# Performance work log

Hardware: AMD Instinct MI355X
Metric: run time of the kernel (lower is better)

The kernel has to match this reference:

```python
import jax, jax.numpy as jnp
import numpy as np

NUM_TAGS = 128
NUM_FEATURES = 500000
B, T, F = 64, 512, 8


def setup_inputs() -> dict:
    key = jax.random.key(0)
    ks = jax.random.split(key, 6)
    feats = jax.random.randint(ks[0], (B, T, F), 0, NUM_FEATURES)
    tags = jax.random.randint(ks[1], (B, T), 0, NUM_TAGS)
    # original init: uniform(-0.01, 0.01)
    state_weights = jax.random.uniform(ks[2], (NUM_TAGS, NUM_FEATURES), minval=-0.01, maxval=0.01, dtype=jnp.float32)
    transitions = jax.random.uniform(ks[3], (NUM_TAGS, NUM_TAGS), minval=-0.01, maxval=0.01, dtype=jnp.float32)
    start_transitions = jax.random.uniform(ks[4], (NUM_TAGS,), minval=-0.01, maxval=0.01, dtype=jnp.float32)
    end_transitions = jax.random.uniform(ks[5], (NUM_TAGS,), minval=-0.01, maxval=0.01, dtype=jnp.float32)
    return dict(feats=feats, tags=tags, state_weights=state_weights,
                transitions=transitions, start_transitions=start_transitions,
                end_transitions=end_transitions)


def reference(feats, tags, state_weights, transitions, start_transitions, end_transitions):
    """Batched CRF negative log-likelihood per sentence: logZ - gold_score. Returns [B]."""
    # emissions[b,t,k] = sum_f state_weights[k, feats[b,t,f]]  (emissions_for_sentence)
    emissions = jnp.take(state_weights, feats, axis=1).sum(-1)   # [K,B,T]
    emissions = jnp.moveaxis(emissions, 0, -1)                    # [B,T,K]

    # log_partition: forward algorithm over T via scan
    alpha0 = start_transitions[None, :] + emissions[:, 0]         # [B,K]

    def step(alpha, em_t):
        # scores[b,i,j] = alpha[b,i] + transitions[i,j]
        scores = alpha[:, :, None] + transitions[None, :, :]
        return jax.nn.logsumexp(scores, axis=1) + em_t, None

    em_rest = jnp.moveaxis(emissions[:, 1:], 1, 0)                # [T-1,B,K]
    alphaT, _ = jax.lax.scan(step, alpha0, em_rest)
    log_z = jax.nn.logsumexp(alphaT + end_transitions[None, :], axis=1)   # [B]

    # gold_score, vectorized over batch
    em_gold = jnp.take_along_axis(emissions, tags[..., None], axis=2)[..., 0].sum(axis=1)  # [B]
    trans_gold = transitions[tags[:, :-1], tags[:, 1:]].sum(axis=1)                        # [B]
    gold = start_transitions[tags[:, 0]] + end_transitions[tags[:, -1]] + em_gold + trans_gold

    return log_z - gold
```

## Files before the change

kernel.cpp:

```cpp
#include <hip/hip_runtime.h>

#define NUM_TAGS 128
#define NUM_FEATS 500000
#define BB 64
#define TT 512
#define FF 8

#define SWT_BYTES 128000000ull
#define EM_BYTES  16777216ull
#define NEED_FULL (SWT_BYTES + EM_BYTES)

typedef __attribute__((ext_vector_type(8))) short short8;
typedef __attribute__((ext_vector_type(4))) float float4v;

__device__ inline unsigned short f2bf(float f) {
  unsigned u = __float_as_uint(f);
  return (unsigned short)((u + 0x7fffu + ((u >> 16) & 1u)) >> 16);
}
__device__ inline float bf2f(unsigned short h) {
  return __uint_as_float(((unsigned)h) << 16);
}

__global__ __launch_bounds__(256) void transpose_kernel(
    const float* __restrict__ sw, unsigned short* __restrict__ swT) {
  __shared__ float tile[32][129];
  const int f0 = blockIdx.x * 32;
  const int t = threadIdx.x;
  const int fi = t & 31, kb = t >> 5;
#pragma unroll
  for (int it = 0; it < 16; ++it) {
    int k = kb + it * 8;
    tile[fi][k] = sw[(size_t)k * NUM_FEATS + f0 + fi];
  }
  __syncthreads();
  const int kp = (t & 63) * 2, fo = t >> 6;
#pragma unroll
  for (int it = 0; it < 8; ++it) {
    int f2 = fo + it * 4;
    unsigned v = (unsigned)f2bf(tile[f2][kp]) |
                 ((unsigned)f2bf(tile[f2][kp + 1]) << 16);
    *(unsigned*)&swT[(size_t)(f0 + f2) * NUM_TAGS + kp] = v;
  }
}

__global__ __launch_bounds__(128) void gather_t_kernel(
    const int* __restrict__ feats, const unsigned short* __restrict__ swT,
    float* __restrict__ em_exp) {
  const int token = blockIdx.x;
  const int k = threadIdx.x;
  const int* f = feats + token * FF;
  float s = 0.f;
#pragma unroll
  for (int i = 0; i < FF; ++i) s += bf2f(swT[(size_t)f[i] * NUM_TAGS + k]);
  em_exp[(size_t)token * NUM_TAGS + k] = __expf(s);
}

__global__ __launch_bounds__(128) void gather_f_kernel(
    const int* __restrict__ feats, const float* __restrict__ sw,
    float* __restrict__ em_exp) {
  const int token = blockIdx.x;
  const int k = threadIdx.x;
  const int* f = feats + token * FF;
  const float* row = sw + (size_t)k * NUM_FEATS;
  float s = 0.f;
#pragma unroll
  for (int i = 0; i < FF; ++i) s += row[f[i]];
  em_exp[(size_t)token * NUM_TAGS + k] = __expf(s);
}

#define NB 16
#define LROW 136
#define LBUF (NB * LROW)

__global__ __launch_bounds__(256, 1) void fwd_kernel(
    const float* __restrict__ em_exp, const int* __restrict__ tags,
    const float* __restrict__ trans, const float* __restrict__ startT,
    const float* __restrict__ endT, float* __restrict__ out) {
  __shared__ __align__(16) unsigned short abuf[2][LBUF];
  __shared__ float red[16][17];

  const int tid = threadIdx.x;
  const int bl = tid & 15;
  const int h = (tid >> 4) & 3;
  const int w = tid >> 6;
  const int bg = blockIdx.x * NB + bl;

  short8 afrag[2][4];
#pragma unroll
  for (int mt = 0; mt < 2; ++mt) {
    const int j = (2 * w + mt) * 16 + bl;
#pragma unroll
    for (int kc = 0; kc < 4; ++kc) {
      short8 a;
#pragma unroll
      for (int jj = 0; jj < 8; ++jj) {
        int i = kc * 32 + h * 8 + jj;
        a[jj] = (short)f2bf(__expf(trans[i * NUM_TAGS + j]) * 0.0078125f);
      }
      afrag[mt][kc] = a;
    }
  }

  const float* emb = em_exp + (size_t)bg * TT * NUM_TAGS;

  {
    const int jc = tid >> 4, j0 = jc * 8;
#pragma unroll
    for (int jj = 0; jj < 8; ++jj)
      abuf[0][bl * LROW + j0 + jj] =
          f2bf(__expf(startT[j0 + jj]) * emb[j0 + jj]);
  }
  __syncthreads();

  float4v ev[2];
#pragma unroll
  for (int mt = 0; mt < 2; ++mt) {
    int j0 = (2 * w + mt) * 16 + h * 4;
    ev[mt] = *(const float4v*)&emb[(size_t)NUM_TAGS + j0];
  }

  for (int t = 1; t < TT; ++t) {
    const unsigned short* cur = abuf[(t - 1) & 1];
    unsigned short* nxt = abuf[t & 1];

    short8 bfrag[4];
#pragma unroll
    for (int kc = 0; kc < 4; ++kc)
      bfrag[kc] = *(const short8*)&cur[bl * LROW + kc * 32 + h * 8];

    float4v acc0 = {0.f, 0.f, 0.f, 0.f}, acc1 = {0.f, 0.f, 0.f, 0.f};
#pragma unroll
    for (int kc = 0; kc < 4; ++kc) {
      acc0 = __builtin_amdgcn_mfma_f32_16x16x32_bf16(afrag[0][kc], bfrag[kc], acc0, 0, 0, 0);
      acc1 = __builtin_amdgcn_mfma_f32_16x16x32_bf16(afrag[1][kc], bfrag[kc], acc1, 0, 0, 0);
    }

    float4v e0 = ev[0], e1 = ev[1];
    if (t + 1 < TT) {
#pragma unroll
      for (int mt = 0; mt < 2; ++mt) {
        int j0 = (2 * w + mt) * 16 + h * 4;
        ev[mt] = *(const float4v*)&emb[(size_t)(t + 1) * NUM_TAGS + j0];
      }
    }
    {
      int j0 = (2 * w + 0) * 16 + h * 4;
      uint2 u;
      u.x = (unsigned)f2bf(acc0[0] * e0[0]) | ((unsigned)f2bf(acc0[1] * e0[1]) << 16);
      u.y = (unsigned)f2bf(acc0[2] * e0[2]) | ((unsigned)f2bf(acc0[3] * e0[3]) << 16);
      *(uint2*)&nxt[bl * LROW + j0] = u;
    }
    {
      int j0 = (2 * w + 1) * 16 + h * 4;
      uint2 u;
      u.x = (unsigned)f2bf(acc1[0] * e1[0]) | ((unsigned)f2bf(acc1[1] * e1[1]) << 16);
      u.y = (unsigned)f2bf(acc1[2] * e1[2]) | ((unsigned)f2bf(acc1[3] * e1[3]) << 16);
      *(uint2*)&nxt[bl * LROW + j0] = u;
    }
    __syncthreads();
  }

  {
    const int jc = tid >> 4, j0 = jc * 8;
    const unsigned short* fin = abuf[(TT - 1) & 1];
    float val = 0.f;
#pragma unroll
    for (int jj = 0; jj < 8; ++jj)
      val += bf2f(fin[bl * LROW + j0 + jj]) * __expf(endT[j0 + jj]);
    red[jc][bl] = val;
  }
  __syncthreads();
  float logzv = 0.f;
  if (tid < 16) {
    float s = 0.f;
#pragma unroll
    for (int q = 0; q < 16; ++q) s += red[q][tid];
    logzv = __logf(s) + 511.0f * 7.0f * 0.69314718055994531f;
  }
  __syncthreads();

  {
    const int seg = tid >> 4;
    const int* tb = tags + (size_t)bg * TT;
    float g = 0.f;
    for (int t = seg * 32; t < seg * 32 + 32; ++t) {
      int tg = tb[t];
      g += __logf(emb[(size_t)t * NUM_TAGS + tg]);
      if (t < TT - 1) g += trans[tg * NUM_TAGS + tb[t + 1]];
    }
    if (seg == 0) g += startT[tb[0]];
    if (seg == 15) g += endT[tb[TT - 1]];
    red[seg][bl] = g;
  }
  __syncthreads();
  if (tid < 16) {
    float s = 0.f;
#pragma unroll
    for (int q = 0; q < 16; ++q) s += red[q][tid];
    out[blockIdx.x * NB + tid] = logzv - s;
  }
}

extern "C" void kernel_launch(void* const* d_in, const int* in_sizes, int n_in,
                              void* d_out, int out_size, void* d_ws, size_t ws_size,
                              hipStream_t stream) {
  const int* feats = (const int*)d_in[0];
  const int* tags = (const int*)d_in[1];
  const float* sw = (const float*)d_in[2];
  const float* trans = (const float*)d_in[3];
  const float* startT = (const float*)d_in[4];
  const float* endT = (const float*)d_in[5];
  float* out = (float*)d_out;

  if (ws_size >= NEED_FULL) {
    unsigned short* swT = (unsigned short*)d_ws;
    float* em_exp = (float*)((char*)d_ws + SWT_BYTES);
    transpose_kernel<<<NUM_FEATS / 32, 256, 0, stream>>>(sw, swT);
    gather_t_kernel<<<BB * TT, 128, 0, stream>>>(feats, swT, em_exp);
    fwd_kernel<<<BB / NB, 256, 0, stream>>>(em_exp, tags, trans, startT, endT, out);
  } else {
    float* em_exp = (float*)d_ws;
    gather_f_kernel<<<BB * TT, 128, 0, stream>>>(feats, sw, em_exp);
    fwd_kernel<<<BB / NB, 256, 0, stream>>>(em_exp, tags, trans, startT, endT, out);
  }
}
```

Baseline: 633.9 us.

## Run CRF forward recursion in one wave with bf16 emissions and vectorized transpose

The forward recursion now runs entirely in a single wavefront that holds all eight MFMA tiles, so the per-timestep __syncthreads across four waves and the LDS double buffer go away. A second wave computes the gold score at the same time. Emissions are stored as bf16 instead of fp32, halving their write and read traffic. The transpose now uses float4 loads, and the gather packs two tags per lane with four tokens per block. Risks are lower emission precision, a longer serial MFMA chain per step in one wave, and cheaper round-to-nearest without ties-to-even in the recurrence.

```diff
diff --git a/kernel.cpp b/kernel.cpp
--- a/kernel.cpp
+++ b/kernel.cpp
@@ -7,7 +7,7 @@
 #define FF 8
 
 #define SWT_BYTES 128000000ull
-#define EM_BYTES  16777216ull
+#define EM_BYTES  (64ull * 512 * 128 * 2)
 #define NEED_FULL (SWT_BYTES + EM_BYTES)
 
 typedef __attribute__((ext_vector_type(8))) short short8;
@@ -23,182 +23,187 @@
 
 __global__ __launch_bounds__(256) void transpose_kernel(
     const float* __restrict__ sw, unsigned short* __restrict__ swT) {
-  __shared__ float tile[32][129];
+  __shared__ float tile[128][33];
   const int f0 = blockIdx.x * 32;
   const int t = threadIdx.x;
-  const int fi = t & 31, kb = t >> 5;
-#pragma unroll
-  for (int it = 0; it < 16; ++it) {
-    int k = kb + it * 8;
-    tile[fi][k] = sw[(size_t)k * NUM_FEATS + f0 + fi];
+  const int c = t & 7, kr = t >> 3;
+#pragma unroll
+  for (int p = 0; p < 4; ++p) {
+    int k = kr + 32 * p;
+    float4 v = *(const float4*)&sw[(size_t)k * NUM_FEATS + f0 + 4 * c];
+    tile[k][4 * c + 0] = v.x; tile[k][4 * c + 1] = v.y;
+    tile[k][4 * c + 2] = v.z; tile[k][4 * c + 3] = v.w;
   }
   __syncthreads();
-  const int kp = (t & 63) * 2, fo = t >> 6;
-#pragma unroll
-  for (int it = 0; it < 8; ++it) {
-    int f2 = fo + it * 4;
-    unsigned v = (unsigned)f2bf(tile[f2][kp]) |
-                 ((unsigned)f2bf(tile[f2][kp + 1]) << 16);
-    *(unsigned*)&swT[(size_t)(f0 + f2) * NUM_TAGS + kp] = v;
-  }
-}
-
-__global__ __launch_bounds__(128) void gather_t_kernel(
+  const int l = t & 63, fr = t >> 6;
+#pragma unroll
+  for (int p = 0; p < 8; ++p) {
+    int f = fr + 4 * p;
+    unsigned lo = f2bf(tile[2 * l][f]);
+    unsigned hi = f2bf(tile[2 * l + 1][f]);
+    *(unsigned*)&swT[(size_t)(f0 + f) * NUM_TAGS + 2 * l] = lo | (hi << 16);
+  }
+}
+
+__global__ __launch_bounds__(256) void gather_kernel(
     const int* __restrict__ feats, const unsigned short* __restrict__ swT,
-    float* __restrict__ em_exp) {
-  const int token = blockIdx.x;
-  const int k = threadIdx.x;
+    unsigned short* __restrict__ em) {
+  const int w = threadIdx.x >> 6, lane = threadIdx.x & 63;
+  const int token = blockIdx.x * 4 + w;
   const int* f = feats + token * FF;
-  float s = 0.f;
-#pragma unroll
-  for (int i = 0; i < FF; ++i) s += bf2f(swT[(size_t)f[i] * NUM_TAGS + k]);
-  em_exp[(size_t)token * NUM_TAGS + k] = __expf(s);
-}
-
-__global__ __launch_bounds__(128) void gather_f_kernel(
+  int fi[FF];
+#pragma unroll
+  for (int i = 0; i < FF; ++i) fi[i] = f[i];
+  float s0 = 0.f, s1 = 0.f;
+#pragma unroll
+  for (int i = 0; i < FF; ++i) {
+    unsigned u = *(const unsigned*)&swT[(size_t)fi[i] * NUM_TAGS + 2 * lane];
+    s0 += __uint_as_float(u << 16);
+    s1 += __uint_as_float(u & 0xFFFF0000u);
+  }
+  unsigned lo = f2bf(__expf(s0));
+  unsigned hi = f2bf(__expf(s1));
+  *(unsigned*)&em[(size_t)token * NUM_TAGS + 2 * lane] = lo | (hi << 16);
+}
+
+__global__ __launch_bounds__(256) void gather_f_kernel(
     const int* __restrict__ feats, const float* __restrict__ sw,
-    float* __restrict__ em_exp) {
-  const int token = blockIdx.x;
-  const int k = threadIdx.x;
+    unsigned short* __restrict__ em) {
+  const int w = threadIdx.x >> 6, lane = threadIdx.x & 63;
+  const int token = blockIdx.x * 4 + w;
   const int* f = feats + token * FF;
-  const float* row = sw + (size_t)k * NUM_FEATS;
-  float s = 0.f;
-#pragma unroll
-  for (int i = 0; i < FF; ++i) s += row[f[i]];
-  em_exp[(size_t)token * NUM_TAGS + k] = __expf(s);
+  float s0 = 0.f, s1 = 0.f;
+#pragma unroll
+  for (int i = 0; i < FF; ++i) {
+    s0 += sw[(size_t)(2 * lane) * NUM_FEATS + f[i]];
+    s1 += sw[(size_t)(2 * lane + 1) * NUM_FEATS + f[i]];
+  }
+  unsigned lo = f2bf(__expf(s0));
+  unsigned hi = f2bf(__expf(s1));
+  *(unsigned*)&em[(size_t)token * NUM_TAGS + 2 * lane] = lo | (hi << 16);
 }
 
 #define NB 16
 #define LROW 136
-#define LBUF (NB * LROW)
-
-__global__ __launch_bounds__(256, 1) void fwd_kernel(
-    const float* __restrict__ em_exp, const int* __restrict__ tags,
+
+__global__ __launch_bounds__(128, 1) void fwd_kernel(
+    const unsigned short* __restrict__ em, const int* __restrict__ tags,
     const float* __restrict__ trans, const float* __restrict__ startT,
     const float* __restrict__ endT, float* __restrict__ out) {
-  __shared__ __align__(16) unsigned short abuf[2][LBUF];
-  __shared__ float red[16][17];
+  __shared__ __align__(16) unsigned short alds[NB * LROW];
+  __shared__ float redz[NB], redg[NB];
 
   const int tid = threadIdx.x;
-  const int bl = tid & 15;
-  const int h = (tid >> 4) & 3;
-  const int w = tid >> 6;
-  const int bg = blockIdx.x * NB + bl;
-
-  short8 afrag[2][4];
-#pragma unroll
-  for (int mt = 0; mt < 2; ++mt) {
-    const int j = (2 * w + mt) * 16 + bl;
-#pragma unroll
-    for (int kc = 0; kc < 4; ++kc) {
-      short8 a;
-#pragma unroll
-      for (int jj = 0; jj < 8; ++jj) {
-        int i = kc * 32 + h * 8 + jj;
-        a[jj] = (short)f2bf(__expf(trans[i * NUM_TAGS + j]) * 0.0078125f);
-      }
-      afrag[mt][kc] = a;
-    }
-  }
-
-  const float* emb = em_exp + (size_t)bg * TT * NUM_TAGS;
-
-  {
-    const int jc = tid >> 4, j0 = jc * 8;
-#pragma unroll
-    for (int jj = 0; jj < 8; ++jj)
-      abuf[0][bl * LROW + j0 + jj] =
-          f2bf(__expf(startT[j0 + jj]) * emb[j0 + jj]);
-  }
+  const int wav = tid >> 6, lane = tid & 63;
+  const int bl = lane & 15, h = lane >> 4;
+  const int b0 = blockIdx.x * NB;
+
+  if (wav == 0) {
+    short8 afrag[8][4];
+#pragma unroll
+    for (int mt = 0; mt < 8; ++mt) {
+      const int j = mt * 16 + bl;
+#pragma unroll
+      for (int kc = 0; kc < 4; ++kc) {
+        short8 a;
+#pragma unroll
+        for (int jj = 0; jj < 8; ++jj) {
+          int i = kc * 32 + h * 8 + jj;
+          a[jj] = (short)f2bf(__expf(trans[i * NUM_TAGS + j]) * 0.0078125f);
+        }
+        afrag[mt][kc] = a;
+      }
+    }
+
+    const unsigned short* emb = em + (size_t)(b0 + bl) * TT * NUM_TAGS;
+
+#pragma unroll
+    for (int mt = 0; mt < 8; ++mt)
+#pragma unroll
+      for (int r = 0; r < 4; ++r) {
+        int j = 16 * mt + 4 * h + r;
+        alds[bl * LROW + j] = f2bf(__expf(startT[j]) * bf2f(emb[j]));
+      }
+
+    uint2 evb[8];
+#pragma unroll
+    for (int mt = 0; mt < 8; ++mt)
+      evb[mt] = *(const uint2*)&emb[(size_t)1 * NUM_TAGS + 16 * mt + 4 * h];
+
+    for (int t = 1; t < TT; ++t) {
+      short8 bfrag[4];
+#pragma unroll
+      for (int kc = 0; kc < 4; ++kc)
+        bfrag[kc] = *(const short8*)&alds[bl * LROW + kc * 32 + h * 8];
+
+      float4v acc[8];
+#pragma unroll
+      for (int mt = 0; mt < 8; ++mt) acc[mt] = (float4v){0.f, 0.f, 0.f, 0.f};
+#pragma unroll
+      for (int kc = 0; kc < 4; ++kc)
+#pragma unroll
+        for (int mt = 0; mt < 8; ++mt)
+          acc[mt] = __builtin_amdgcn_mfma_f32_16x16x32_bf16(
+              afrag[mt][kc], bfrag[kc], acc[mt], 0, 0, 0);
+
+      uint2 evn[8];
+      if (t + 1 < TT) {
+#pragma unroll
+        for (int mt = 0; mt < 8; ++mt)
+          evn[mt] = *(const uint2*)&emb[(size_t)(t + 1) * NUM_TAGS + 16 * mt + 4 * h];
+      }
+
+#pragma unroll
+      for (int mt = 0; mt < 8; ++mt) {
+        float e0 = __uint_as_float(evb[mt].x << 16);
+        float e1 = __uint_as_float(evb[mt].x & 0xFFFF0000u);
+        float e2 = __uint_as_float(evb[mt].y << 16);
+        float e3 = __uint_as_float(evb[mt].y & 0xFFFF0000u);
+        unsigned a0 = __float_as_uint(acc[mt][0] * e0) + 0x8000u;
+        unsigned a1 = __float_as_uint(acc[mt][1] * e1) + 0x8000u;
+        unsigned a2 = __float_as_uint(acc[mt][2] * e2) + 0x8000u;
+        unsigned a3 = __float_as_uint(acc[mt][3] * e3) + 0x8000u;
+        uint2 o;
+        o.x = __builtin_amdgcn_perm(a1, a0, 0x07060302u);
+        o.y = __builtin_amdgcn_perm(a3, a2, 0x07060302u);
+        *(uint2*)&alds[bl * LROW + 16 * mt + 4 * h] = o;
+      }
+#pragma unroll
+      for (int mt = 0; mt < 8; ++mt) evb[mt] = evn[mt];
+    }
+
+    {
+      const int bb = lane >> 2, q = lane & 3;
+      float sum = 0.f;
+      for (int j = 32 * q; j < 32 * q + 32; ++j)
+        sum += bf2f(alds[bb * LROW + j]) * __expf(endT[j]);
+      sum += __shfl_xor(sum, 1, 64);
+      sum += __shfl_xor(sum, 2, 64);
+      if (q == 0) redz[bb] = __logf(sum) + 511.0f * 7.0f * 0.69314718055994531f;
+    }
+  } else {
+    const int bb = lane >> 2, seg = lane & 3;
+    const int* tb = tags + (size_t)(b0 + bb) * TT;
+    const unsigned short* emb = em + (size_t)(b0 + bb) * TT * NUM_TAGS;
+    float g = 0.f;
+    int tg = tb[seg * 128];
+    for (int t = seg * 128; t < seg * 128 + 128; ++t) {
+      g += __logf(bf2f(emb[(size_t)t * NUM_TAGS + tg]));
+      if (t < TT - 1) {
+        int tn = tb[t + 1];
+        g += trans[tg * NUM_TAGS + tn];
+        tg = tn;
+      }
+    }
+    if (seg == 0) g += startT[tb[0]];
+    if (seg == 3) g += endT[tb[TT - 1]];
+    g += __shfl_xor(g, 1, 64);
+    g += __shfl_xor(g, 2, 64);
+    if (seg == 0) redg[bb] = g;
+  }
+
   __syncthreads();
-
-  float4v ev[2];
-#pragma unroll
-  for (int mt = 0; mt < 2; ++mt) {
-    int j0 = (2 * w + mt) * 16 + h * 4;
-    ev[mt] = *(const float4v*)&emb[(size_t)NUM_TAGS + j0];
-  }
-
-  for (int t = 1; t < TT; ++t) {
-    const unsigned short* cur = abuf[(t - 1) & 1];
-    unsigned short* nxt = abuf[t & 1];
-
-    short8 bfrag[4];
-#pragma unroll
-    for (int kc = 0; kc < 4; ++kc)
-      bfrag[kc] = *(const short8*)&cur[bl * LROW + kc * 32 + h * 8];
-
-    float4v acc0 = {0.f, 0.f, 0.f, 0.f}, acc1 = {0.f, 0.f, 0.f, 0.f};
-#pragma unroll
-    for (int kc = 0; kc < 4; ++kc) {
-      acc0 = __builtin_amdgcn_mfma_f32_16x16x32_bf16(afrag[0][kc], bfrag[kc], acc0, 0, 0, 0);
-      acc1 = __builtin_amdgcn_mfma_f32_16x16x32_bf16(afrag[1][kc], bfrag[kc], acc1, 0, 0, 0);
-    }
-
-    float4v e0 = ev[0], e1 = ev[1];
-    if (t + 1 < TT) {
-#pragma unroll
-      for (int mt = 0; mt < 2; ++mt) {
-        int j0 = (2 * w + mt) * 16 + h * 4;
-        ev[mt] = *(const float4v*)&emb[(size_t)(t + 1) * NUM_TAGS + j0];
-      }
-    }
-    {
-      int j0 = (2 * w + 0) * 16 + h * 4;
-      uint2 u;
-      u.x = (unsigned)f2bf(acc0[0] * e0[0]) | ((unsigned)f2bf(acc0[1] * e0[1]) << 16);
-      u.y = (unsigned)f2bf(acc0[2] * e0[2]) | ((unsigned)f2bf(acc0[3] * e0[3]) << 16);
-      *(uint2*)&nxt[bl * LROW + j0] = u;
-    }
-    {
-      int j0 = (2 * w + 1) * 16 + h * 4;
-      uint2 u;
-      u.x = (unsigned)f2bf(acc1[0] * e1[0]) | ((unsigned)f2bf(acc1[1] * e1[1]) << 16);
-      u.y = (unsigned)f2bf(acc1[2] * e1[2]) | ((unsigned)f2bf(acc1[3] * e1[3]) << 16);
-      *(uint2*)&nxt[bl * LROW + j0] = u;
-    }
-    __syncthreads();
-  }
-
-  {
-    const int jc = tid >> 4, j0 = jc * 8;
-    const unsigned short* fin = abuf[(TT - 1) & 1];
-    float val = 0.f;
-#pragma unroll
-    for (int jj = 0; jj < 8; ++jj)
-      val += bf2f(fin[bl * LROW + j0 + jj]) * __expf(endT[j0 + jj]);
-    red[jc][bl] = val;
-  }
-  __syncthreads();
-  float logzv = 0.f;
-  if (tid < 16) {
-    float s = 0.f;
-#pragma unroll
-    for (int q = 0; q < 16; ++q) s += red[q][tid];
-    logzv = __logf(s) + 511.0f * 7.0f * 0.69314718055994531f;
-  }
-  __syncthreads();
-
-  {
-    const int seg = tid >> 4;
-    const int* tb = tags + (size_t)bg * TT;
-    float g = 0.f;
-    for (int t = seg * 32; t < seg * 32 + 32; ++t) {
-      int tg = tb[t];
-      g += __logf(emb[(size_t)t * NUM_TAGS + tg]);
-      if (t < TT - 1) g += trans[tg * NUM_TAGS + tb[t + 1]];
-    }
-    if (seg == 0) g += startT[tb[0]];
-    if (seg == 15) g += endT[tb[TT - 1]];
-    red[seg][bl] = g;
-  }
-  __syncthreads();
-  if (tid < 16) {
-    float s = 0.f;
-#pragma unroll
-    for (int q = 0; q < 16; ++q) s += red[q][tid];
-    out[blockIdx.x * NB + tid] = logzv - s;
-  }
+  if (tid < NB) out[b0 + tid] = redz[tid] - redg[tid];
 }
 
 extern "C" void kernel_launch(void* const* d_in, const int* in_sizes, int n_in,
@@ -214,13 +219,13 @@
 
   if (ws_size >= NEED_FULL) {
     unsigned short* swT = (unsigned short*)d_ws;
-    float* em_exp = (float*)((char*)d_ws + SWT_BYTES);
+    unsigned short* em = (unsigned short*)((char*)d_ws + SWT_BYTES);
     transpose_kernel<<<NUM_FEATS / 32, 256, 0, stream>>>(sw, swT);
-    gather_t_kernel<<<BB * TT, 128, 0, stream>>>(feats, swT, em_exp);
-    fwd_kernel<<<BB / NB, 256, 0, stream>>>(em_exp, tags, trans, startT, endT, out);
+    gather_kernel<<<BB * TT / 4, 256, 0, stream>>>(feats, swT, em);
+    fwd_kernel<<<BB / NB, 128, 0, stream>>>(em, tags, trans, startT, endT, out);
   } else {
-    float* em_exp = (float*)d_ws;
-    gather_f_kernel<<<BB * TT, 128, 0, stream>>>(feats, sw, em_exp);
-    fwd_kernel<<<BB / NB, 256, 0, stream>>>(em_exp, tags, trans, startT, endT, out);
-  }
-}
+    unsigned short* em = (unsigned short*)d_ws;
+    gather_f_kernel<<<BB * TT / 4, 256, 0, stream>>>(feats, sw, em);
+    fwd_kernel<<<BB / NB, 128, 0, stream>>>(em, tags, trans, startT, endT, out);
+  }
+}
```

Result: slower. 712.0 us (+12.3%).
